# Optimization experiments

Measured on AMD Instinct MI355X. Metric: run time of the kernel, lower is better.

The kernel has to match this reference:

```python
import jax, jax.numpy as jnp
import numpy as np

B, S, HID = 1, 2048, 4096
NH, NKV, HD = 32, 8, 128
WINDOW = 1024
ROPE_THETA = 1e6
NEG = -1e9


def rotate_half(x):
    x1, x2 = jnp.split(x, 2, axis=-1)
    return jnp.concatenate((-x2, x1), axis=-1)


def setup_inputs() -> dict:
    key = jax.random.key(0)
    ks = jax.random.split(key, 10)
    hidden_states = jax.random.normal(ks[0], (B, S, HID), jnp.float32)
    # rotary tables [max_pos, head_dim]
    inv_freq = 1.0 / (ROPE_THETA ** (jnp.arange(0, HD, 2, dtype=jnp.float32) / HD))
    t = jnp.arange(S, dtype=jnp.float32)
    freqs = jnp.outer(t, inv_freq)                       # [S, HD/2]
    emb = jnp.concatenate((freqs, freqs), axis=-1)       # [S, HD]
    cos, sin = jnp.cos(emb), jnp.sin(emb)
    position_ids = jnp.arange(S, dtype=jnp.int64)[None, :].astype(jnp.int32)
    # sliding-window causal additive mask [B,1,S,S]
    i = jnp.arange(S)[:, None]
    j = jnp.arange(S)[None, :]
    allowed = (j <= i) & (j > i - WINDOW)
    attention_mask = jnp.where(allowed, 0.0, NEG).astype(jnp.float32)[None, None]
    sc = 0.02
    Wq = jax.random.normal(ks[1], (HID, NH * HD), jnp.float32) * sc
    bq = jax.random.normal(ks[2], (NH * HD,), jnp.float32) * sc
    Wk = jax.random.normal(ks[3], (HID, NKV * HD), jnp.float32) * sc
    bk = jax.random.normal(ks[4], (NKV * HD,), jnp.float32) * sc
    Wv = jax.random.normal(ks[5], (HID, NKV * HD), jnp.float32) * sc
    bv = jax.random.normal(ks[6], (NKV * HD,), jnp.float32) * sc
    Wo = jax.random.normal(ks[7], (NH * HD, HID), jnp.float32) * sc
    bo = jax.random.normal(ks[8], (HID,), jnp.float32) * sc
    return dict(hidden_states=hidden_states, attention_mask=attention_mask,
                position_ids=position_ids, cos=cos, sin=sin,
                Wq=Wq, bq=bq, Wk=Wk, bk=bk, Wv=Wv, bv=bv, Wo=Wo, bo=bo)


def reference(hidden_states, attention_mask, position_ids, cos, sin,
              Wq, bq, Wk, bk, Wv, bv, Wo, bo):
    bsz, q_len, _ = hidden_states.shape
    q = (hidden_states @ Wq + bq).reshape(bsz, q_len, NH, HD).transpose(0, 2, 1, 3)
    k = (hidden_states @ Wk + bk).reshape(bsz, q_len, NKV, HD).transpose(0, 2, 1, 3)
    v = (hidden_states @ Wv + bv).reshape(bsz, q_len, NKV, HD).transpose(0, 2, 1, 3)
    # RoPE: cos/sin gathered by position_ids -> [B,1,S,HD]
    c = cos[position_ids][:, None]
    s = sin[position_ids][:, None]
    q = q * c + rotate_half(q) * s
    k = k * c + rotate_half(k) * s
    # GQA repeat_kv: [B,NKV,S,HD] -> [B,NH,S,HD]
    n_rep = NH // NKV
    k = jnp.repeat(k, n_rep, axis=1)
    v = jnp.repeat(v, n_rep, axis=1)
    scores = jnp.einsum('bhqd,bhkd->bhqk', q, k) / np.sqrt(HD).astype(np.float32)
    scores = scores + attention_mask[:, :, :, :k.shape[2]]
    probs = jax.nn.softmax(scores.astype(jnp.float32), axis=-1).astype(q.dtype)
    attn = jnp.einsum('bhqk,bhkd->bhqd', probs, v)
    attn = attn.transpose(0, 2, 1, 3).reshape(bsz, q_len, NH * HD)
    return attn @ Wo + bo
```

## Files before the change

### kernel.cpp

```cpp
#include <hip/hip_runtime.h>
#include <stdint.h>

typedef unsigned short u16;
typedef __attribute__((ext_vector_type(4))) float f32x4;
typedef __attribute__((ext_vector_type(16))) float f32x16;
typedef __attribute__((ext_vector_type(8))) __bf16 bf16x8;
typedef __attribute__((ext_vector_type(4))) u16 u16x4;
typedef __attribute__((ext_vector_type(8))) u16 u16x8;
typedef __attribute__((ext_vector_type(4))) unsigned int u32x4;

#define S_LEN 2048
#define HIDDEN 4096
#define NHEAD 32
#define NKVH 8
#define HD 128
#define WIN 1024

__device__ __forceinline__ float bf2f(u16 u) {
  union { unsigned int i; float f; } x; x.i = ((unsigned int)u) << 16; return x.f;
}
__device__ __forceinline__ u16 f2bf(float f) {
  union { float f; unsigned int i; } x; x.f = f;
  unsigned int r = x.i + 0x7FFFu + ((x.i >> 16) & 1u);
  return (u16)(r >> 16);
}

__device__ __forceinline__ void gload16(const void* g, void* l) {
  __builtin_amdgcn_global_load_lds((const __attribute__((address_space(1))) void*)g,
                                   (__attribute__((address_space(3))) void*)l, 16, 0, 0);
}

__device__ __forceinline__ unsigned int cvtpk_bf16(float a, float b) {
  unsigned int w;
  asm("v_cvt_pk_bf16_f32 %0, %1, %2" : "=v"(w) : "v"(a), "v"(b));
  return w;
}

__device__ __forceinline__ void transp_f32(const float* __restrict__ in, int istride,
                                           u16* __restrict__ out, int ostride,
                                           int bx, int by, char* smem) {
  float (*tile)[68] = (float (*)[68])smem;
  int r0 = bx * 64, c0 = by * 64;
  int t = threadIdx.x;
  int tr = t >> 4;
  int tc = (t & 15) * 4;
#pragma unroll
  for (int i = 0; i < 4; ++i) {
    int r = i * 16 + tr;
    *(f32x4*)&tile[r][tc] = *(const f32x4*)(in + (size_t)(r0 + r) * istride + c0 + tc);
  }
  __syncthreads();
#pragma unroll
  for (int i = 0; i < 4; ++i) {
    int rr = i * 16 + tr;
    u16x4 o;
#pragma unroll
    for (int j = 0; j < 4; ++j) o[j] = f2bf(tile[tc + j][rr]);
    *(u16x4*)(out + (size_t)(c0 + rr) * ostride + r0 + tc) = o;
  }
}

__global__ __launch_bounds__(256) void prep_k(const float* __restrict__ X,
                                              const float* __restrict__ Wq, const float* __restrict__ Wk,
                                              const float* __restrict__ Wv,
                                              const float* __restrict__ bq, const float* __restrict__ bk,
                                              const float* __restrict__ bv,
                                              u16* __restrict__ Xb, u16* __restrict__ WT,
                                              float* __restrict__ bqkv) {
  __shared__ __align__(16) char smem[17408];
  int bid = blockIdx.x;
  if (bid < 4096) {
    size_t i = ((size_t)bid * 256 + threadIdx.x) * 8;
    f32x4 a = *(const f32x4*)(X + i);
    f32x4 b = *(const f32x4*)(X + i + 4);
    u16x8 o;
    o[0] = f2bf(a[0]); o[1] = f2bf(a[1]); o[2] = f2bf(a[2]); o[3] = f2bf(a[3]);
    o[4] = f2bf(b[0]); o[5] = f2bf(b[1]); o[6] = f2bf(b[2]); o[7] = f2bf(b[3]);
    *(u16x8*)(Xb + i) = o;
  } else if (bid < 8192) {
    int tt = bid - 4096;
    transp_f32(Wq, 4096, WT, 4096, tt & 63, tt >> 6, smem);
  } else if (bid < 9216) {
    int tt = bid - 8192;
    transp_f32(Wk, 1024, WT + (size_t)4096 * 4096, 4096, tt & 63, tt >> 6, smem);
  } else if (bid < 10240) {
    int tt = bid - 9216;
    transp_f32(Wv, 1024, WT + (size_t)5120 * 4096, 4096, tt & 63, tt >> 6, smem);
  } else {
    int i = (bid - 10240) * 256 + threadIdx.x;
    float v = (i < 4096) ? bq[i] : (i < 5120 ? bk[i - 4096] : bv[i - 5120]);
    bqkv[i] = v;
  }
}

__global__ __launch_bounds__(256) void mid_k(const u16* __restrict__ qkv, const int* __restrict__ pos,
                                             const float* __restrict__ cosT, const float* __restrict__ sinT,
                                             u16* __restrict__ Q, u16* __restrict__ Kf, u16* __restrict__ Vf,
                                             const float* __restrict__ Wo, u16* __restrict__ WT) {
  __shared__ __align__(16) char smem[17408];
  int bid = blockIdx.x;
  if (bid < 20480) {
    int p = bid * 256 + threadIdx.x;
    int s = p / 2560;
    int rem = p - s * 2560;
    int hs = rem >> 6;
    int d = rem & 63;
    int ps = pos[s];
    const float* cb = cosT + (size_t)ps * 128;
    const float* sb = sinT + (size_t)ps * 128;
    float c0 = cb[d], c1 = cb[d + 64], s0 = sb[d], s1 = sb[d + 64];
    if (hs < NHEAD) {
      const u16* src = qkv + (size_t)s * 6144 + hs * 128;
      float x0 = bf2f(src[d]), x1 = bf2f(src[d + 64]);
      const float qs = 0.08838834764831845f;
      u16* dst = Q + ((size_t)hs * S_LEN + s) * HD;
      dst[d] = f2bf((x0 * c0 - x1 * s0) * qs);
      dst[d + 64] = f2bf((x1 * c1 + x0 * s1) * qs);
    } else {
      int kh = hs - NHEAD;
      const u16* src = qkv + (size_t)s * 6144 + 4096 + kh * 128;
      float x0 = bf2f(src[d]), x1 = bf2f(src[d + 64]);
      int t = s >> 5, cr = s & 31;
      int ks = d >> 4, hi2 = (d >> 3) & 1, j = d & 7;
      size_t base = ((size_t)(kh * 64 + t) * 8 + ks) * 512 + (size_t)(cr + 32 * hi2) * 8 + j;
      Kf[base] = f2bf(x0 * c0 - x1 * s0);
      Kf[base + 4 * 512] = f2bf(x1 * c1 + x0 * s1);
    }
  } else if (bid < 20992) {
    u16 (*tile)[136] = (u16 (*)[136])smem;
    int b2 = bid - 20480;
    int kh = b2 >> 6, t = b2 & 63;
    int tid = threadIdx.x;
#pragma unroll
    for (int i = 0; i < 2; ++i) {
      int c = tid + i * 256;
      int r = c >> 4, seg = c & 15;
      *(u16x8*)&tile[r][seg * 8] =
          *(const u16x8*)(qkv + (size_t)(t * 32 + r) * 6144 + 5120 + kh * 128 + seg * 8);
    }
    __syncthreads();
#pragma unroll
    for (int i = 0; i < 2; ++i) {
      int pp = tid + i * 256;
      int dt = pp >> 7, sl = (pp >> 6) & 1, l = pp & 63;
      int c2 = l & 31, h2 = l >> 5;
      u16x8 o;
#pragma unroll
      for (int j = 0; j < 8; ++j) o[j] = tile[sl * 16 + h2 * 8 + j][dt * 32 + c2];
      *(u16x8*)(Vf + ((size_t)(kh * 512 + t * 8 + dt * 2 + sl)) * 512 + (size_t)l * 8) = o;
    }
  } else {
    int tt = bid - 20992;
    transp_f32(Wo, 4096, WT, 4096, tt & 63, tt >> 6, smem);
  }
}

template <int BM, int BN, int MINW, typename TOUT>
__global__ __launch_bounds__(256, MINW) void gemm4_k(const u16* __restrict__ A, const u16* __restrict__ Bt,
                                                     const float* __restrict__ bias, TOUT* __restrict__ C,
                                                     int M, int N, int K) {
  constexpr int WM = BM / 2, WN = BN / 2;
  constexpr int MRA = WM / 16, MRB = WN / 16;
  constexpr int NA = BM / 64, NB = BN / 64;
  constexpr int NL = NA + NB;
  __shared__ __align__(16) u16 SA[3 * BM * 32];
  __shared__ __align__(16) u16 SB[3 * BN * 32];

  int tid = threadIdx.x;
  int w = tid >> 6, l = tid & 63;
  int cl = l & 15, g = l >> 4;
  int wr = w >> 1, wc = w & 1;

  int cpx = gridDim.x >> 3;
  int wg = (blockIdx.x & 7) * cpx + (blockIdx.x >> 3);
  int nbm = M / BM;
  int bm = wg % nbm, bn = wg / nbm;

  const u16* Ag = A + (size_t)(bm * BM) * K;
  const u16* Bg = Bt + (size_t)(bn * BN) * K;
  int srow = w * 16 + (l >> 2);
  int csrc = ((l & 3) ^ ((l >> 3) & 3)) * 8;
  int rdc = (g ^ ((cl >> 1) & 3)) << 3;

  f32x4 acc[MRA][MRB] = {};
  int NT = K >> 5;

  auto stage = [&](int slot, int tt, int h) {
    if (h < NA) {
      gload16(Ag + (size_t)(h * 64 + srow) * K + tt * 32 + csrc,
              (void*)(SA + slot * (BM * 32) + (h * 64 + w * 16) * 32));
    } else {
      int hb = h - NA;
      gload16(Bg + (size_t)(hb * 64 + srow) * K + tt * 32 + csrc,
              (void*)(SB + slot * (BN * 32) + (hb * 64 + w * 16) * 32));
    }
  };

#pragma unroll
  for (int h = 0; h < NL; ++h) stage(0, 0, h);
#pragma unroll
  for (int h = 0; h < NL; ++h) stage(1, 1, h);

  for (int t = 0; t < NT; ++t) {
    if constexpr (NL == 5) asm volatile("s_waitcnt vmcnt(5)" ::: "memory");
    else if constexpr (NL == 4) asm volatile("s_waitcnt vmcnt(4)" ::: "memory");
    else asm volatile("s_waitcnt vmcnt(3)" ::: "memory");
    __builtin_amdgcn_s_barrier();
    asm volatile("" ::: "memory");

    int slot = t % 3, ss = (t + 2) % 3;
    int ts = t + 2; if (ts >= NT) ts -= NT;
#pragma unroll
    for (int h = 0; h < NL; ++h) stage(ss, ts, h);

    const u16* sa = SA + slot * (BM * 32);
    const u16* sb = SB + slot * (BN * 32);
    bf16x8 af[MRA], bf[MRB];
#pragma unroll
    for (int mi = 0; mi < MRA; ++mi)
      af[mi] = *(const bf16x8*)(sa + (wr * WM + mi * 16 + cl) * 32 + rdc);
#pragma unroll
    for (int ni = 0; ni < MRB; ++ni)
      bf[ni] = *(const bf16x8*)(sb + (wc * WN + ni * 16 + cl) * 32 + rdc);
    __builtin_amdgcn_s_setprio(1);
#pragma unroll
    for (int mi = 0; mi < MRA; ++mi)
#pragma unroll
      for (int ni = 0; ni < MRB; ++ni)
        acc[mi][ni] = __builtin_amdgcn_mfma_f32_16x16x32_bf16(af[mi], bf[ni], acc[mi][ni], 0, 0, 0);
    __builtin_amdgcn_s_setprio(0);
  }

  asm volatile("s_waitcnt vmcnt(0)" ::: "memory");

#pragma unroll
  for (int mi = 0; mi < MRA; ++mi) {
    int row0 = bm * BM + wr * WM + mi * 16 + g * 4;
#pragma unroll
    for (int ni = 0; ni < MRB; ++ni) {
      int col = bn * BN + wc * WN + ni * 16 + cl;
      float bb = bias[col];
      f32x4 a = acc[mi][ni];
#pragma unroll
      for (int r = 0; r < 4; ++r) {
        float v = a[r] + bb;
        if constexpr (sizeof(TOUT) == 2) C[(size_t)(row0 + r) * N + col] = f2bf(v);
        else C[(size_t)(row0 + r) * N + col] = v;
      }
    }
  }
}

__global__ __launch_bounds__(256, 2) void attn_k(const u16* __restrict__ Q, const u16* __restrict__ Kf,
                                                 const u16* __restrict__ Vf, u16* __restrict__ O) {
  int l = threadIdx.x & 63, w = threadIdx.x >> 6;
  int col = l & 31, hi = l >> 5;
  int bid = blockIdx.x;
  int kh = bid & 7;
  int head = (bid >> 3) & 3;
  int qbp = bid >> 5;
  int qb = (qbp & 1) ? (15 - (qbp >> 1)) : (qbp >> 1);
  int h = kh * 4 + head;
  int q0 = qb * 128 + w * 32;

  bf16x8 qf[8];
  const u16* qbase = Q + ((size_t)h * S_LEN + q0 + col) * HD + hi * 8;
#pragma unroll
  for (int ks = 0; ks < 8; ++ks) qf[ks] = *(const bf16x8*)(qbase + ks * 16);

  f32x16 ot[4];
#pragma unroll
  for (int dt = 0; dt < 4; ++dt)
#pragma unroll
    for (int r = 0; r < 16; ++r) ot[dt][r] = 0.f;
  float m_r = -3.0e38f, l_r = 0.f;

  const u16* kf0 = Kf + (size_t)kh * 64 * 4096 + (size_t)l * 8;
  const u16* vf0 = Vf + (size_t)kh * 512 * 512 + (size_t)l * 8;

  int jstart = q0 >= WIN ? q0 - WIN : 0;
  bf16x8 kfr[8];
  {
    const u16* kb = kf0 + (size_t)(jstart >> 5) * 4096;
#pragma unroll
    for (int ks = 0; ks < 8; ++ks) kfr[ks] = *(const bf16x8*)(kb + ks * 512);
  }

  for (int j0 = jstart; j0 <= q0; j0 += 32) {
    int t = j0 >> 5;
    f32x16 sA = {}, sB = {};
#pragma unroll
    for (int ks = 0; ks < 4; ++ks)
      sA = __builtin_amdgcn_mfma_f32_32x32x16_bf16(kfr[ks], qf[ks], sA, 0, 0, 0);
#pragma unroll
    for (int ks = 4; ks < 8; ++ks)
      sB = __builtin_amdgcn_mfma_f32_32x32x16_bf16(kfr[ks], qf[ks], sB, 0, 0, 0);
    int tn = (j0 + 32 <= q0) ? (t + 1) : t;
    const u16* kbn = kf0 + (size_t)tn * 4096;
    bf16x8 kfn[8];
#pragma unroll
    for (int ks = 0; ks < 8; ++ks) kfn[ks] = *(const bf16x8*)(kbn + ks * 512);
    const u16* vb = vf0 + (size_t)t * 4096;
    bf16x8 vfr[8];
#pragma unroll
    for (int c = 0; c < 8; ++c) vfr[c] = *(const bf16x8*)(vb + c * 512);

    f32x16 s = sA + sB;

    if (j0 + 31 > q0 || j0 < q0 - 992) {
      int q = q0 + col;
#pragma unroll
      for (int r = 0; r < 16; ++r) {
        int kv = j0 + (r & 3) + 8 * (r >> 2) + 4 * hi;
        if (kv > q || kv <= q - WIN) s[r] = -3.0e38f;
      }
    }
    float vm = fmaxf(fmaxf(fmaxf(s[0], s[1]), fmaxf(s[2], s[3])),
                     fmaxf(fmaxf(s[4], s[5]), fmaxf(s[6], s[7])));
    vm = fmaxf(vm, fmaxf(fmaxf(fmaxf(s[8], s[9]), fmaxf(s[10], s[11])),
                         fmaxf(fmaxf(s[12], s[13]), fmaxf(s[14], s[15]))));
    vm = fmaxf(vm, __shfl_xor(vm, 32));
    float mnew = fmaxf(m_r, vm);
    float sc = __expf(m_r - mnew);
    m_r = mnew;
    float rs = 0.f;
#pragma unroll
    for (int r = 0; r < 16; ++r) {
      float pv = __expf(s[r] - mnew);
      s[r] = pv;
      rs += pv;
    }
    rs += __shfl_xor(rs, 32);
    l_r = l_r * sc + rs;
#pragma unroll
    for (int dt = 0; dt < 4; ++dt)
#pragma unroll
      for (int r = 0; r < 16; ++r) ot[dt][r] *= sc;

    bf16x8 pb[2];
#pragma unroll
    for (int sl = 0; sl < 2; ++sl) {
      int b = sl * 8;
      unsigned int a0 = cvtpk_bf16(s[b + 0], s[b + 1]);
      unsigned int c0 = cvtpk_bf16(s[b + 4], s[b + 5]);
      asm("v_permlane32_swap_b32 %0, %1" : "+v"(a0), "+v"(c0));
      unsigned int a1 = cvtpk_bf16(s[b + 2], s[b + 3]);
      unsigned int c1 = cvtpk_bf16(s[b + 6], s[b + 7]);
      asm("v_permlane32_swap_b32 %0, %1" : "+v"(a1), "+v"(c1));
      u32x4 pv = {a0, a1, c0, c1};
      pb[sl] = __builtin_bit_cast(bf16x8, pv);
    }
#pragma unroll
    for (int dt = 0; dt < 4; ++dt) {
      ot[dt] = __builtin_amdgcn_mfma_f32_32x32x16_bf16(vfr[dt * 2 + 0], pb[0], ot[dt], 0, 0, 0);
      ot[dt] = __builtin_amdgcn_mfma_f32_32x32x16_bf16(vfr[dt * 2 + 1], pb[1], ot[dt], 0, 0, 0);
    }
#pragma unroll
    for (int ks = 0; ks < 8; ++ks) kfr[ks] = kfn[ks];
  }

  float inv = 1.0f / l_r;
#pragma unroll
  for (int dt = 0; dt < 4; ++dt) {
#pragma unroll
    for (int g2 = 0; g2 < 4; ++g2) {
      u16x4 o;
#pragma unroll
      for (int i = 0; i < 4; ++i) o[i] = f2bf(ot[dt][g2 * 4 + i] * inv);
      *(u16x4*)(O + (size_t)(q0 + col) * HIDDEN + h * HD + dt * 32 + g2 * 8 + hi * 4) = o;
    }
  }
}

extern "C" void kernel_launch(void* const* d_in, const int* in_sizes, int n_in,
                              void* d_out, int out_size, void* d_ws, size_t ws_size,
                              hipStream_t stream) {
  const float* X = (const float*)d_in[0];
  const int* pos = (const int*)d_in[2];
  const float* cosT = (const float*)d_in[3];
  const float* sinT = (const float*)d_in[4];
  const float* Wq = (const float*)d_in[5];
  const float* bq = (const float*)d_in[6];
  const float* Wk = (const float*)d_in[7];
  const float* bk = (const float*)d_in[8];
  const float* Wv = (const float*)d_in[9];
  const float* bv = (const float*)d_in[10];
  const float* Wo = (const float*)d_in[11];
  const float* bo = (const float*)d_in[12];
  float* out = (float*)d_out;

  const size_t MB = 1ull << 20;
  char* ws = (char*)d_ws;
  u16* WT = (u16*)ws;
  u16* Xb = (u16*)(ws + 48 * MB);
  u16* Qs = Xb;
  u16* QKVr = (u16*)(ws + 64 * MB);
  u16* attnO = QKVr;
  u16* Kfr = (u16*)(ws + 88 * MB);
  u16* Vfr = (u16*)(ws + 92 * MB);
  float* bqkv = (float*)(ws + 96 * MB);

  prep_k<<<10264, 256, 0, stream>>>(X, Wq, Wk, Wv, bq, bk, bv, Xb, WT, bqkv);

  gemm4_k<128, 128, 3, u16><<<768, 256, 0, stream>>>(Xb, WT, bqkv, QKVr, 2048, 6144, 4096);

  mid_k<<<25088, 256, 0, stream>>>(QKVr, pos, cosT, sinT, Qs, Kfr, Vfr, Wo, WT);

  attn_k<<<512, 256, 0, stream>>>(Qs, Kfr, Vfr, attnO);

  gemm4_k<128, 128, 3, float><<<512, 256, 0, stream>>>(attnO, WT, bo, out, 2048, 4096, 4096);
}
```

Measured before the change: 329.5 us.

## Fuse RoPE and K/V relayout into QKV GEMM epilogue; fold Wo transpose into attention

The QKV projection GEMM now stages its output tile through shared memory and applies RoPE, Q scaling and the K/V fragment relayouts directly in its epilogue. This removes the separate mid kernel and the round trip of the intermediate QKV buffer through global memory. The Wo transpose-and-convert blocks are appended to the attention launch so they can overlap with attention work. The cost is a heavier epilogue and extra shared-memory staging in the GEMM, and attention blocks now share the device with the transpose blocks.

```diff
diff --git a/kernel.cpp b/kernel.cpp
--- a/kernel.cpp
+++ b/kernel.cpp
@@ -93,65 +93,161 @@
   }
 }
 
-__global__ __launch_bounds__(256) void mid_k(const u16* __restrict__ qkv, const int* __restrict__ pos,
-                                             const float* __restrict__ cosT, const float* __restrict__ sinT,
-                                             u16* __restrict__ Q, u16* __restrict__ Kf, u16* __restrict__ Vf,
-                                             const float* __restrict__ Wo, u16* __restrict__ WT) {
-  __shared__ __align__(16) char smem[17408];
-  int bid = blockIdx.x;
-  if (bid < 20480) {
-    int p = bid * 256 + threadIdx.x;
-    int s = p / 2560;
-    int rem = p - s * 2560;
-    int hs = rem >> 6;
-    int d = rem & 63;
+__global__ __launch_bounds__(256, 3) void gemmqkv_k(const u16* __restrict__ A, const u16* __restrict__ Bt,
+                                                    const float* __restrict__ bias,
+                                                    const int* __restrict__ pos,
+                                                    const float* __restrict__ cosT, const float* __restrict__ sinT,
+                                                    u16* __restrict__ Q, u16* __restrict__ Kf,
+                                                    u16* __restrict__ Vf, int K) {
+  constexpr int NL = 4;
+  __shared__ __align__(16) u16 SM[24576];
+  u16* SA = SM;
+  u16* SB = SM + 12288;
+
+  int tid = threadIdx.x;
+  int w = tid >> 6, l = tid & 63;
+  int cl = l & 15, g = l >> 4;
+  int wr = w >> 1, wc = w & 1;
+
+  int cpx = gridDim.x >> 3;
+  int wg = (blockIdx.x & 7) * cpx + (blockIdx.x >> 3);
+  int bm = wg & 15, bn = wg >> 4;
+
+  const u16* Ag = A + (size_t)(bm * 128) * K;
+  const u16* Bg = Bt + (size_t)(bn * 128) * K;
+  int srow = w * 16 + (l >> 2);
+  int csrc = ((l & 3) ^ ((l >> 3) & 3)) * 8;
+  int rdc = (g ^ ((cl >> 1) & 3)) << 3;
+
+  f32x4 acc[4][4] = {};
+  int NT = K >> 5;
+
+  auto stage = [&](int slot, int tt, int h) {
+    if (h < 2) {
+      gload16(Ag + (size_t)(h * 64 + srow) * K + tt * 32 + csrc,
+              (void*)(SA + slot * 4096 + (h * 64 + w * 16) * 32));
+    } else {
+      int hb = h - 2;
+      gload16(Bg + (size_t)(hb * 64 + srow) * K + tt * 32 + csrc,
+              (void*)(SB + slot * 4096 + (hb * 64 + w * 16) * 32));
+    }
+  };
+
+#pragma unroll
+  for (int h = 0; h < NL; ++h) stage(0, 0, h);
+#pragma unroll
+  for (int h = 0; h < NL; ++h) stage(1, 1, h);
+
+  for (int t = 0; t < NT; ++t) {
+    asm volatile("s_waitcnt vmcnt(4)" ::: "memory");
+    __builtin_amdgcn_s_barrier();
+    asm volatile("" ::: "memory");
+
+    int slot = t % 3, ss = (t + 2) % 3;
+    int ts = t + 2; if (ts >= NT) ts -= NT;
+#pragma unroll
+    for (int h = 0; h < NL; ++h) stage(ss, ts, h);
+
+    const u16* sa = SA + slot * 4096;
+    const u16* sb = SB + slot * 4096;
+    bf16x8 af[4], bf[4];
+#pragma unroll
+    for (int mi = 0; mi < 4; ++mi)
+      af[mi] = *(const bf16x8*)(sa + (wr * 64 + mi * 16 + cl) * 32 + rdc);
+#pragma unroll
+    for (int ni = 0; ni < 4; ++ni)
+      bf[ni] = *(const bf16x8*)(sb + (wc * 64 + ni * 16 + cl) * 32 + rdc);
+    __builtin_amdgcn_s_setprio(1);
+#pragma unroll
+    for (int mi = 0; mi < 4; ++mi)
+#pragma unroll
+      for (int ni = 0; ni < 4; ++ni)
+        acc[mi][ni] = __builtin_amdgcn_mfma_f32_16x16x32_bf16(af[mi], bf[ni], acc[mi][ni], 0, 0, 0);
+    __builtin_amdgcn_s_setprio(0);
+  }
+
+  asm volatile("s_waitcnt vmcnt(0)" ::: "memory");
+  __syncthreads();
+
+  u16 (*tileL)[132] = (u16 (*)[132])SM;
+#pragma unroll
+  for (int mi = 0; mi < 4; ++mi)
+#pragma unroll
+    for (int ni = 0; ni < 4; ++ni) {
+      int col = wc * 64 + ni * 16 + cl;
+      float bb = bias[bn * 128 + col];
+#pragma unroll
+      for (int r = 0; r < 4; ++r)
+        tileL[wr * 64 + mi * 16 + g * 4 + r][col] = f2bf(acc[mi][ni][r] + bb);
+    }
+  __syncthreads();
+
+  int s0 = bm * 128;
+  if (bn < 32) {
+    int hq = bn;
+    int r = tid >> 1, u = tid & 1;
+    int s = s0 + r;
     int ps = pos[s];
     const float* cb = cosT + (size_t)ps * 128;
     const float* sb = sinT + (size_t)ps * 128;
-    float c0 = cb[d], c1 = cb[d + 64], s0 = sb[d], s1 = sb[d + 64];
-    if (hs < NHEAD) {
-      const u16* src = qkv + (size_t)s * 6144 + hs * 128;
-      float x0 = bf2f(src[d]), x1 = bf2f(src[d + 64]);
-      const float qs = 0.08838834764831845f;
-      u16* dst = Q + ((size_t)hs * S_LEN + s) * HD;
-      dst[d] = f2bf((x0 * c0 - x1 * s0) * qs);
-      dst[d + 64] = f2bf((x1 * c1 + x0 * s1) * qs);
-    } else {
-      int kh = hs - NHEAD;
-      const u16* src = qkv + (size_t)s * 6144 + 4096 + kh * 128;
-      float x0 = bf2f(src[d]), x1 = bf2f(src[d + 64]);
-      int t = s >> 5, cr = s & 31;
-      int ks = d >> 4, hi2 = (d >> 3) & 1, j = d & 7;
-      size_t base = ((size_t)(kh * 64 + t) * 8 + ks) * 512 + (size_t)(cr + 32 * hi2) * 8 + j;
-      Kf[base] = f2bf(x0 * c0 - x1 * s0);
-      Kf[base + 4 * 512] = f2bf(x1 * c1 + x0 * s1);
-    }
-  } else if (bid < 20992) {
-    u16 (*tile)[136] = (u16 (*)[136])smem;
-    int b2 = bid - 20480;
-    int kh = b2 >> 6, t = b2 & 63;
-    int tid = threadIdx.x;
-#pragma unroll
-    for (int i = 0; i < 2; ++i) {
-      int c = tid + i * 256;
-      int r = c >> 4, seg = c & 15;
-      *(u16x8*)&tile[r][seg * 8] =
-          *(const u16x8*)(qkv + (size_t)(t * 32 + r) * 6144 + 5120 + kh * 128 + seg * 8);
-    }
-    __syncthreads();
-#pragma unroll
-    for (int i = 0; i < 2; ++i) {
-      int pp = tid + i * 256;
-      int dt = pp >> 7, sl = (pp >> 6) & 1, l = pp & 63;
-      int c2 = l & 31, h2 = l >> 5;
+    u16* dst = Q + ((size_t)hq * S_LEN + s) * HD;
+    const float qs = 0.08838834764831845f;
+#pragma unroll
+    for (int c8 = 0; c8 < 4; ++c8) {
+      int d0 = u * 32 + c8 * 8;
+      u16x8 lo, hi;
+#pragma unroll
+      for (int j = 0; j < 8; ++j) {
+        int d = d0 + j;
+        float x0 = bf2f(tileL[r][d]);
+        float x1 = bf2f(tileL[r][d + 64]);
+        lo[j] = f2bf((x0 * cb[d] - x1 * sb[d]) * qs);
+        hi[j] = f2bf((x1 * cb[d + 64] + x0 * sb[d + 64]) * qs);
+      }
+      *(u16x8*)(dst + d0) = lo;
+      *(u16x8*)(dst + d0 + 64) = hi;
+    }
+  } else if (bn < 40) {
+    int kh = bn - 32;
+    int r = tid >> 1, u = tid & 1;
+    int s = s0 + r;
+    int ps = pos[s];
+    const float* cb = cosT + (size_t)ps * 128;
+    const float* sb = sinT + (size_t)ps * 128;
+    int t2 = s >> 5, cr = s & 31;
+#pragma unroll
+    for (int c8 = 0; c8 < 4; ++c8) {
+      int d0 = u * 32 + c8 * 8;
+      u16x8 lo, hi;
+#pragma unroll
+      for (int j = 0; j < 8; ++j) {
+        int d = d0 + j;
+        float x0 = bf2f(tileL[r][d]);
+        float x1 = bf2f(tileL[r][d + 64]);
+        lo[j] = f2bf(x0 * cb[d] - x1 * sb[d]);
+        hi[j] = f2bf(x1 * cb[d + 64] + x0 * sb[d + 64]);
+      }
+      size_t base_lo = ((size_t)(kh * 64 + t2) * 8 + (d0 >> 4)) * 512 + (size_t)(cr + 32 * ((d0 >> 3) & 1)) * 8;
+      *(u16x8*)(Kf + base_lo) = lo;
+      int dh = d0 + 64;
+      size_t base_hi = ((size_t)(kh * 64 + t2) * 8 + (dh >> 4)) * 512 + (size_t)(cr + 32 * ((dh >> 3) & 1)) * 8;
+      *(u16x8*)(Kf + base_hi) = hi;
+    }
+  } else {
+    int kh = bn - 40;
+#pragma unroll
+    for (int i = 0; i < 8; ++i) {
+      int c = i * 256 + tid;
+      int lv = c & 63, sl = (c >> 6) & 1, dt = (c >> 7) & 3, t2l = c >> 9;
+      int h2 = lv >> 5, c2 = lv & 31;
+      int rl = t2l * 32 + sl * 16 + h2 * 8;
+      int colv = dt * 32 + c2;
       u16x8 o;
 #pragma unroll
-      for (int j = 0; j < 8; ++j) o[j] = tile[sl * 16 + h2 * 8 + j][dt * 32 + c2];
-      *(u16x8*)(Vf + ((size_t)(kh * 512 + t * 8 + dt * 2 + sl)) * 512 + (size_t)l * 8) = o;
-    }
-  } else {
-    int tt = bid - 20992;
-    transp_f32(Wo, 4096, WT, 4096, tt & 63, tt >> 6, smem);
+      for (int j = 0; j < 8; ++j) o[j] = tileL[rl + j][colv];
+      size_t addr = ((size_t)(kh * 512 + (bm * 4 + t2l) * 8 + dt * 2 + sl)) * 512 + (size_t)lv * 8;
+      *(u16x8*)(Vf + addr) = o;
+    }
   }
 }
 
@@ -251,8 +347,15 @@
   }
 }
 
-__global__ __launch_bounds__(256, 2) void attn_k(const u16* __restrict__ Q, const u16* __restrict__ Kf,
-                                                 const u16* __restrict__ Vf, u16* __restrict__ O) {
+__global__ __launch_bounds__(256, 2) void attnwot_k(const u16* __restrict__ Q, const u16* __restrict__ Kf,
+                                                    const u16* __restrict__ Vf, u16* __restrict__ O,
+                                                    const float* __restrict__ Wo, u16* __restrict__ WT) {
+  __shared__ __align__(16) char smem[17408];
+  if (blockIdx.x >= 512) {
+    int tt = blockIdx.x - 512;
+    transp_f32(Wo, 4096, WT, 4096, tt & 63, tt >> 6, smem);
+    return;
+  }
   int l = threadIdx.x & 63, w = threadIdx.x >> 6;
   int col = l & 31, hi = l >> 5;
   int bid = blockIdx.x;
@@ -393,20 +496,17 @@
   char* ws = (char*)d_ws;
   u16* WT = (u16*)ws;
   u16* Xb = (u16*)(ws + 48 * MB);
-  u16* Qs = Xb;
-  u16* QKVr = (u16*)(ws + 64 * MB);
-  u16* attnO = QKVr;
+  u16* attnO = Xb;
+  u16* Qs = (u16*)(ws + 64 * MB);
   u16* Kfr = (u16*)(ws + 88 * MB);
   u16* Vfr = (u16*)(ws + 92 * MB);
   float* bqkv = (float*)(ws + 96 * MB);
 
   prep_k<<<10264, 256, 0, stream>>>(X, Wq, Wk, Wv, bq, bk, bv, Xb, WT, bqkv);
 
-  gemm4_k<128, 128, 3, u16><<<768, 256, 0, stream>>>(Xb, WT, bqkv, QKVr, 2048, 6144, 4096);
-
-  mid_k<<<25088, 256, 0, stream>>>(QKVr, pos, cosT, sinT, Qs, Kfr, Vfr, Wo, WT);
-
-  attn_k<<<512, 256, 0, stream>>>(Qs, Kfr, Vfr, attnO);
+  gemmqkv_k<<<768, 256, 0, stream>>>(Xb, WT, bqkv, pos, cosT, sinT, Qs, Kfr, Vfr, 4096);
+
+  attnwot_k<<<4608, 256, 0, stream>>>(Qs, Kfr, Vfr, attnO, Wo, WT);
 
   gemm4_k<128, 128, 3, float><<<512, 256, 0, stream>>>(attnO, WT, bo, out, 2048, 4096, 4096);
 }
```

Result: faster. 321.1 us (-2.6%).
